# Kernel tuning notes

Measured on AMD Instinct MI355X. Metric: run time of the kernel, lower is better.

Reference implementation:

```python
import jax, jax.numpy as jnp
import numpy as np

VOCAB, EMBED = 100000, 128
B, QLEN, DLEN = 1024, 32, 256
KERNEL_NUM, SIGMA, EXACT_SIGMA = 11, 0.1, 0.001
EPS = 1e-8  # torch F.cosine_similarity eps


def _kernel_mus(n):
    l_mu = [1.0]
    if n == 1:
        return l_mu
    bin_size = 2.0 / (n - 1)
    l_mu.append(1 - bin_size / 2)
    for i in range(1, n - 1):
        l_mu.append(round(l_mu[i] - bin_size, 5))
    return list(reversed(l_mu))


def _kernel_sigmas(n, sigma, exact_sigma):
    l_sigma = [exact_sigma]
    if n == 1:
        return l_sigma
    l_sigma += [sigma] * (n - 1)
    return list(reversed(l_sigma))


MUS = jnp.asarray(np.array(_kernel_mus(KERNEL_NUM), dtype=np.float32))      # [K]
SIGMAS = jnp.asarray(np.array(_kernel_sigmas(KERNEL_NUM, SIGMA, EXACT_SIGMA), dtype=np.float32))  # [K]


def setup_inputs() -> dict:
    key = jax.random.key(0)
    k = jax.random.split(key, 7)
    return {
        "emb": jax.random.normal(k[0], (VOCAB, EMBED), dtype=jnp.float32),
        "mlp_w": jax.random.normal(k[1], (1, KERNEL_NUM), dtype=jnp.float32) * 0.3,
        "mlp_b": jax.random.normal(k[2], (1,), dtype=jnp.float32) * 0.1,
        "query1": jax.random.randint(k[3], (B, QLEN), 0, VOCAB, dtype=jnp.int32).astype(jnp.int64),
        "doc1": jax.random.randint(k[4], (B, DLEN), 0, VOCAB, dtype=jnp.int32).astype(jnp.int64),
        "query2": jax.random.randint(k[5], (B, QLEN), 0, VOCAB, dtype=jnp.int32).astype(jnp.int64),
        "doc2": jax.random.randint(k[6], (B, DLEN), 0, VOCAB, dtype=jnp.int32).astype(jnp.int64),
    }


def _predict(emb, mlp_w, mlp_b, query, doc):
    qe = emb[query]                               # [B,Q,E]
    de = emb[doc]                                 # [B,D,E]
    qn = jnp.linalg.norm(qe, axis=-1)             # [B,Q]
    dn = jnp.linalg.norm(de, axis=-1)             # [B,D]
    dots = jnp.einsum("bqe,bde->bqd", qe, de)    # [B,Q,D]
    sim = dots / jnp.maximum(qn[:, :, None] * dn[:, None, :], EPS)
    # multi-Gaussian soft histogram: exp(-(sim-mu)^2/(2 sigma^2)), sum over doc,
    # log1p, sum over query  -> [B,K]
    z = (sim[..., None] - MUS) / SIGMAS           # [B,Q,D,K]
    K = jnp.exp(-0.5 * z * z)
    pooled = jnp.log1p(K.sum(axis=2)).sum(axis=1)  # [B,K]
    return pooled @ mlp_w.T + mlp_b               # [B,1]


def reference(emb, mlp_w, mlp_b, query1, doc1, query2, doc2):
    logits_1 = _predict(emb, mlp_w, mlp_b, query1, doc1)
    logits_2 = _predict(emb, mlp_w, mlp_b, query2, doc2)
    return jax.nn.sigmoid(logits_1 - logits_2)    # [B,1]
```

## Files before the change

kernel.cpp:

```cpp
#include <hip/hip_runtime.h>
#include <math.h>

#define VOCAB 100000
#define NB    1024
#define QLEN  32
#define DLEN  256
#define EMBED 128
#define KNUM  11

typedef __attribute__((ext_vector_type(8))) short bf16x8;
typedef __attribute__((ext_vector_type(4))) float f32x4;

#define HALF_L2E 0.7213475204444817f
#define TWO_L2E  2.8853900817779268f
#define EM4      0.018315638888734179f

#define SSTR 66
#define SREG (32 * SSTR)

__global__ __launch_bounds__(256)
void cvt_table(const float* __restrict__ emb, ushort* __restrict__ ebf,
               float* __restrict__ inorm)
{
    const int row  = blockIdx.x * 4 + (threadIdx.x >> 6);
    const int lane = threadIdx.x & 63;
    const float2 v = *((const float2*)(emb + (size_t)row * EMBED) + lane);
    union { float f; unsigned u; } a, b;
    a.f = v.x; b.f = v.y;
    const unsigned ra = a.u + 0x8000u;
    const unsigned rb = b.u + 0x8000u;
    *((unsigned*)(ebf + (size_t)row * EMBED) + lane) = (ra >> 16) | (rb & 0xFFFF0000u);
    a.u = ra & 0xFFFF0000u; b.u = rb & 0xFFFF0000u;
    float n = a.f * a.f + b.f * b.f;
    #pragma unroll
    for (int m = 1; m < 64; m <<= 1) n += __shfl_xor(n, m);
    if (lane == 0) inorm[row] = __builtin_amdgcn_rsqf(n);
}

__device__ __forceinline__ bf16x8 cvt8(const float* p, float& nacc)
{
    uint4 a = *((const uint4*)p);
    uint4 b = *((const uint4*)(p + 4));
    unsigned u[8] = {a.x, a.y, a.z, a.w, b.x, b.y, b.z, b.w};
    bf16x8 r;
    #pragma unroll
    for (int i = 0; i < 8; ++i) {
        const unsigned q = u[i] + 0x8000u;
        r[i] = (short)(q >> 16);
        union { unsigned uu; float ff; } g; g.uu = q & 0xFFFF0000u;
        nacc = fmaf(g.ff, g.ff, nacc);
    }
    return r;
}

template<bool PRE>
__global__ __launch_bounds__(256)
void knrm_logits(const float* __restrict__ emb,
                 const ushort* __restrict__ ebf,
                 const float* __restrict__ inorm,
                 const float* __restrict__ mlp_w,
                 const int* __restrict__ q1, const int* __restrict__ d1,
                 const int* __restrict__ q2, const int* __restrict__ d2,
                 float* __restrict__ logits)
{
    const int b    = blockIdx.x;
    const int pair = blockIdx.y;
    const int t    = threadIdx.x;
    const int w    = t >> 6;
    const int lane = t & 63;
    const int l15  = lane & 15;
    const int quad = lane >> 4;

    const int* __restrict__ qry = (pair == 0 ? q1 : q2) + b * QLEN;
    const int* __restrict__ doc = (pair == 0 ? d1 : d2) + b * DLEN;

    __shared__ float s_sim[4 * SREG];
    __shared__ float s_part[4][QLEN][KNUM];

    const int qid0 = qry[l15];
    const int qid1 = qry[l15 + 16];
    int did[4];
    #pragma unroll
    for (int nt = 0; nt < 4; ++nt) did[nt] = doc[(w * 4 + nt) * 16 + l15];

    f32x4 acc[2][4];
    #pragma unroll
    for (int mt = 0; mt < 2; ++mt)
        #pragma unroll
        for (int nt = 0; nt < 4; ++nt)
            acc[mt][nt] = (f32x4){0.f, 0.f, 0.f, 0.f};

    float idn[4];
    float riqn[2][4];

    if (PRE) {
        const ushort* qp0 = ebf + (size_t)qid0 * EMBED + quad * 8;
        const ushort* qp1 = ebf + (size_t)qid1 * EMBED + quad * 8;
        #pragma unroll
        for (int kk = 0; kk < 4; ++kk) {
            const bf16x8 a0 = *((const bf16x8*)(qp0 + kk * 32));
            const bf16x8 a1 = *((const bf16x8*)(qp1 + kk * 32));
            #pragma unroll
            for (int nt = 0; nt < 4; ++nt) {
                const bf16x8 bb = *((const bf16x8*)(ebf + (size_t)did[nt] * EMBED + quad * 8 + kk * 32));
                acc[0][nt] = __builtin_amdgcn_mfma_f32_16x16x32_bf16(a0, bb, acc[0][nt], 0, 0, 0);
                acc[1][nt] = __builtin_amdgcn_mfma_f32_16x16x32_bf16(a1, bb, acc[1][nt], 0, 0, 0);
            }
        }
        #pragma unroll
        for (int nt = 0; nt < 4; ++nt) idn[nt] = inorm[did[nt]];
        #pragma unroll
        for (int r = 0; r < 4; ++r) {
            riqn[0][r] = inorm[qry[quad * 4 + r]];
            riqn[1][r] = inorm[qry[16 + quad * 4 + r]];
        }
    } else {
        float qn2[2] = {0.f, 0.f};
        float dn2[4] = {0.f, 0.f, 0.f, 0.f};
        const float* qp0 = emb + (size_t)qid0 * EMBED + quad * 8;
        const float* qp1 = emb + (size_t)qid1 * EMBED + quad * 8;
        #pragma unroll
        for (int kk = 0; kk < 4; ++kk) {
            const bf16x8 a0 = cvt8(qp0 + kk * 32, qn2[0]);
            const bf16x8 a1 = cvt8(qp1 + kk * 32, qn2[1]);
            #pragma unroll
            for (int nt = 0; nt < 4; ++nt) {
                const bf16x8 bb = cvt8(emb + (size_t)did[nt] * EMBED + quad * 8 + kk * 32, dn2[nt]);
                acc[0][nt] = __builtin_amdgcn_mfma_f32_16x16x32_bf16(a0, bb, acc[0][nt], 0, 0, 0);
                acc[1][nt] = __builtin_amdgcn_mfma_f32_16x16x32_bf16(a1, bb, acc[1][nt], 0, 0, 0);
            }
        }
        #pragma unroll
        for (int i = 0; i < 2; ++i) {
            qn2[i] += __shfl_xor(qn2[i], 16);
            qn2[i] += __shfl_xor(qn2[i], 32);
        }
        #pragma unroll
        for (int nt = 0; nt < 4; ++nt) {
            dn2[nt] += __shfl_xor(dn2[nt], 16);
            dn2[nt] += __shfl_xor(dn2[nt], 32);
            idn[nt] = __builtin_amdgcn_rsqf(dn2[nt]);
        }
        #pragma unroll
        for (int r = 0; r < 4; ++r) {
            riqn[0][r] = __builtin_amdgcn_rsqf(__shfl(qn2[0], quad * 4 + r));
            riqn[1][r] = __builtin_amdgcn_rsqf(__shfl(qn2[1], quad * 4 + r));
        }
    }

    {
        float* base = s_sim + w * SREG + (quad * 4) * SSTR + l15;
        #pragma unroll
        for (int mt = 0; mt < 2; ++mt)
            #pragma unroll
            for (int nt = 0; nt < 4; ++nt)
                #pragma unroll
                for (int r = 0; r < 4; ++r)
                    base[(mt * 16 + r) * SSTR + nt * 16] =
                        acc[mt][nt][r] * riqn[mt][r] * idn[nt];
    }
    __syncthreads();

    const int m   = t & 31;
    const int j   = t >> 5;
    const float* rdp = s_sim + (j >> 1) * SREG + m * SSTR + (j & 1);

    float ksum[KNUM];
    #pragma unroll
    for (int k = 0; k < KNUM; ++k) ksum[k] = 0.f;

    #pragma unroll
    for (int i = 0; i < 32; ++i) {
        const float s  = rdp[2 * i];
        const float z  = fmaf(s, 10.f, -1.f);
        const float e0 = exp2f(-HALF_L2E * (z * z));
        float ru = exp2f(fmaf(z,  TWO_L2E, -TWO_L2E));
        float rd = exp2f(fmaf(z, -TWO_L2E, -TWO_L2E));
        ksum[5] += e0;
        float tt = e0;
        tt *= ru; ksum[6] += tt; ru *= EM4;
        tt *= ru; ksum[7] += tt; ru *= EM4;
        tt *= ru; ksum[8] += tt; ru *= EM4;
        tt *= ru; ksum[9] += tt;
        tt = e0;
        tt *= rd; ksum[4] += tt; rd *= EM4;
        tt *= rd; ksum[3] += tt; rd *= EM4;
        tt *= rd; ksum[2] += tt; rd *= EM4;
        tt *= rd; ksum[1] += tt; rd *= EM4;
        tt *= rd; ksum[0] += tt;
        ksum[10] += (s > 0.995f) ? 1.f : 0.f;
    }

    #pragma unroll
    for (int k = 0; k < KNUM; ++k) ksum[k] += __shfl_xor(ksum[k], 32);

    if (lane < 32) {
        #pragma unroll
        for (int k = 0; k < KNUM; ++k) s_part[w][m][k] = ksum[k];
    }
    __syncthreads();

    if (t < QLEN) {
        float contrib = 0.f;
        #pragma unroll
        for (int k = 0; k < KNUM; ++k) {
            const float ks = s_part[0][t][k] + s_part[1][t][k]
                           + s_part[2][t][k] + s_part[3][t][k];
            contrib += mlp_w[k] * log1pf(ks);
        }
        #pragma unroll
        for (int mm = 1; mm < 32; mm <<= 1) contrib += __shfl_xor(contrib, mm);
        if (t == 0) logits[pair * NB + b] = contrib;
    }
}

__global__ __launch_bounds__(256)
void knrm_combine(const float* __restrict__ logits, float* __restrict__ out)
{
    const int i = blockIdx.x * blockDim.x + threadIdx.x;
    if (i < NB) {
        const float d = logits[i] - logits[NB + i];
        out[i] = 1.f / (1.f + __expf(-d));
    }
}

extern "C" void kernel_launch(void* const* d_in, const int* in_sizes, int n_in,
                              void* d_out, int out_size, void* d_ws, size_t ws_size,
                              hipStream_t stream)
{
    const float* emb   = (const float*)d_in[0];
    const float* mlp_w = (const float*)d_in[1];
    const int* q1 = (const int*)d_in[3];
    const int* d1 = (const int*)d_in[4];
    const int* q2 = (const int*)d_in[5];
    const int* d2 = (const int*)d_in[6];

    float* out    = (float*)d_out;
    float* logits = (float*)d_ws;

    const size_t need = 2 * NB * 4
                      + (size_t)VOCAB * 4
                      + (size_t)VOCAB * EMBED * 2 + 256;
    dim3 grid(NB, 2);
    if (ws_size >= need) {
        float*  inorm = logits + 2 * NB;
        ushort* ebf   = (ushort*)(inorm + VOCAB);
        cvt_table<<<VOCAB / 4, 256, 0, stream>>>(emb, ebf, inorm);
        knrm_logits<true><<<grid, 256, 0, stream>>>(emb, ebf, inorm, mlp_w,
                                                    q1, d1, q2, d2, logits);
    } else {
        knrm_logits<false><<<grid, 256, 0, stream>>>(emb, nullptr, nullptr, mlp_w,
                                                     q1, d1, q2, d2, logits);
    }
    knrm_combine<<<(NB + 255) / 256, 256, 0, stream>>>(logits, out);
}
```

Baseline: 146.8 us.

## Shrink similarity LDS tile to per-wave halves and reduce kernels via shared atomics

The main kernel no longer stages the full 32x64 similarity tile per wave. Each wave now writes one 16-row half at a time and evaluates the Gaussian kernels on it straight away. Partial sums are reduced with wave shuffles and LDS atomics into one shared total, which drops the second block-wide barrier over a large tile and cuts LDS use. Together with a launch-bounds occupancy hint, this aims to fit more blocks per CU. The table conversion kernel also now processes 8 rows per block with float4 loads. The costs are an extra barrier to zero the totals, LDS atomic contention, and possible register pressure from the occupancy hint.

```diff
diff --git a/kernel.cpp b/kernel.cpp
--- a/kernel.cpp
+++ b/kernel.cpp
@@ -15,26 +15,30 @@
 #define TWO_L2E  2.8853900817779268f
 #define EM4      0.018315638888734179f
 
-#define SSTR 66
-#define SREG (32 * SSTR)
+#define SSTR  68
+#define SHALF (16 * SSTR)
 
 __global__ __launch_bounds__(256)
 void cvt_table(const float* __restrict__ emb, ushort* __restrict__ ebf,
                float* __restrict__ inorm)
 {
-    const int row  = blockIdx.x * 4 + (threadIdx.x >> 6);
-    const int lane = threadIdx.x & 63;
-    const float2 v = *((const float2*)(emb + (size_t)row * EMBED) + lane);
-    union { float f; unsigned u; } a, b;
-    a.f = v.x; b.f = v.y;
-    const unsigned ra = a.u + 0x8000u;
-    const unsigned rb = b.u + 0x8000u;
-    *((unsigned*)(ebf + (size_t)row * EMBED) + lane) = (ra >> 16) | (rb & 0xFFFF0000u);
-    a.u = ra & 0xFFFF0000u; b.u = rb & 0xFFFF0000u;
-    float n = a.f * a.f + b.f * b.f;
-    #pragma unroll
-    for (int m = 1; m < 64; m <<= 1) n += __shfl_xor(n, m);
-    if (lane == 0) inorm[row] = __builtin_amdgcn_rsqf(n);
+    const int row = blockIdx.x * 8 + (threadIdx.x >> 5);
+    const int l32 = threadIdx.x & 31;
+    const float4 v = *((const float4*)(emb + (size_t)row * EMBED) + l32);
+    union { float f; unsigned u; } x0, x1, x2, x3;
+    x0.f = v.x; x1.f = v.y; x2.f = v.z; x3.f = v.w;
+    const unsigned r0 = x0.u + 0x8000u, r1 = x1.u + 0x8000u;
+    const unsigned r2 = x2.u + 0x8000u, r3 = x3.u + 0x8000u;
+    uint2 packed;
+    packed.x = (r0 >> 16) | (r1 & 0xFFFF0000u);
+    packed.y = (r2 >> 16) | (r3 & 0xFFFF0000u);
+    *((uint2*)(ebf + (size_t)row * EMBED) + l32) = packed;
+    x0.u = r0 & 0xFFFF0000u; x1.u = r1 & 0xFFFF0000u;
+    x2.u = r2 & 0xFFFF0000u; x3.u = r3 & 0xFFFF0000u;
+    float n = x0.f * x0.f + x1.f * x1.f + x2.f * x2.f + x3.f * x3.f;
+    #pragma unroll
+    for (int m = 1; m < 32; m <<= 1) n += __shfl_xor(n, m);
+    if (l32 == 0) inorm[row] = __builtin_amdgcn_rsqf(n);
 }
 
 __device__ __forceinline__ bf16x8 cvt8(const float* p, float& nacc)
@@ -54,7 +58,7 @@
 }
 
 template<bool PRE>
-__global__ __launch_bounds__(256)
+__global__ __launch_bounds__(256, 6)
 void knrm_logits(const float* __restrict__ emb,
                  const ushort* __restrict__ ebf,
                  const float* __restrict__ inorm,
@@ -74,8 +78,12 @@
     const int* __restrict__ qry = (pair == 0 ? q1 : q2) + b * QLEN;
     const int* __restrict__ doc = (pair == 0 ? d1 : d2) + b * DLEN;
 
-    __shared__ float s_sim[4 * SREG];
-    __shared__ float s_part[4][QLEN][KNUM];
+    __shared__ __align__(16) float s_sim[4 * SHALF];
+    __shared__ float s_tot[QLEN][12];
+
+    #pragma unroll
+    for (int i = t; i < QLEN * 12; i += 256) ((float*)s_tot)[i] = 0.f;
+    __syncthreads();
 
     const int qid0 = qry[l15];
     const int qid1 = qry[l15 + 16];
@@ -148,66 +156,68 @@
         }
     }
 
-    {
-        float* base = s_sim + w * SREG + (quad * 4) * SSTR + l15;
-        #pragma unroll
-        for (int mt = 0; mt < 2; ++mt)
-            #pragma unroll
-            for (int nt = 0; nt < 4; ++nt)
-                #pragma unroll
-                for (int r = 0; r < 4; ++r)
-                    base[(mt * 16 + r) * SSTR + nt * 16] =
-                        acc[mt][nt][r] * riqn[mt][r] * idn[nt];
-    }
-    __syncthreads();
-
-    const int m   = t & 31;
-    const int j   = t >> 5;
-    const float* rdp = s_sim + (j >> 1) * SREG + m * SSTR + (j & 1);
-
-    float ksum[KNUM];
-    #pragma unroll
-    for (int k = 0; k < KNUM; ++k) ksum[k] = 0.f;
-
-    #pragma unroll
-    for (int i = 0; i < 32; ++i) {
-        const float s  = rdp[2 * i];
-        const float z  = fmaf(s, 10.f, -1.f);
-        const float e0 = exp2f(-HALF_L2E * (z * z));
-        float ru = exp2f(fmaf(z,  TWO_L2E, -TWO_L2E));
-        float rd = exp2f(fmaf(z, -TWO_L2E, -TWO_L2E));
-        ksum[5] += e0;
-        float tt = e0;
-        tt *= ru; ksum[6] += tt; ru *= EM4;
-        tt *= ru; ksum[7] += tt; ru *= EM4;
-        tt *= ru; ksum[8] += tt; ru *= EM4;
-        tt *= ru; ksum[9] += tt;
-        tt = e0;
-        tt *= rd; ksum[4] += tt; rd *= EM4;
-        tt *= rd; ksum[3] += tt; rd *= EM4;
-        tt *= rd; ksum[2] += tt; rd *= EM4;
-        tt *= rd; ksum[1] += tt; rd *= EM4;
-        tt *= rd; ksum[0] += tt;
-        ksum[10] += (s > 0.995f) ? 1.f : 0.f;
-    }
-
-    #pragma unroll
-    for (int k = 0; k < KNUM; ++k) ksum[k] += __shfl_xor(ksum[k], 32);
-
-    if (lane < 32) {
-        #pragma unroll
-        for (int k = 0; k < KNUM; ++k) s_part[w][m][k] = ksum[k];
+    float* wtile = s_sim + w * SHALF;
+    const int m = l15;
+    const int c = quad;
+
+    #pragma unroll
+    for (int mt = 0; mt < 2; ++mt) {
+        #pragma unroll
+        for (int nt = 0; nt < 4; ++nt)
+            #pragma unroll
+            for (int r = 0; r < 4; ++r)
+                wtile[(quad * 4 + r) * SSTR + nt * 16 + l15] =
+                    acc[mt][nt][r] * riqn[mt][r] * idn[nt];
+
+        const float* rp = wtile + m * SSTR + c * 16;
+        float ksum[KNUM];
+        #pragma unroll
+        for (int k = 0; k < KNUM; ++k) ksum[k] = 0.f;
+
+        #pragma unroll
+        for (int i = 0; i < 4; ++i) {
+            const f32x4 sv = *((const f32x4*)(rp + 4 * i));
+            #pragma unroll
+            for (int e = 0; e < 4; ++e) {
+                const float s  = sv[e];
+                const float z  = fmaf(s, 10.f, -1.f);
+                const float e0 = exp2f(-HALF_L2E * (z * z));
+                float ru = exp2f(fmaf(z,  TWO_L2E, -TWO_L2E));
+                float rd = exp2f(fmaf(z, -TWO_L2E, -TWO_L2E));
+                ksum[5] += e0;
+                float tt = e0;
+                tt *= ru; ksum[6] += tt; ru *= EM4;
+                tt *= ru; ksum[7] += tt; ru *= EM4;
+                tt *= ru; ksum[8] += tt; ru *= EM4;
+                tt *= ru; ksum[9] += tt;
+                tt = e0;
+                tt *= rd; ksum[4] += tt; rd *= EM4;
+                tt *= rd; ksum[3] += tt; rd *= EM4;
+                tt *= rd; ksum[2] += tt; rd *= EM4;
+                tt *= rd; ksum[1] += tt; rd *= EM4;
+                tt *= rd; ksum[0] += tt;
+                ksum[10] += (s > 0.995f) ? 1.f : 0.f;
+            }
+        }
+
+        #pragma unroll
+        for (int k = 0; k < KNUM; ++k) {
+            ksum[k] += __shfl_xor(ksum[k], 16);
+            ksum[k] += __shfl_xor(ksum[k], 32);
+        }
+        if (quad == 0) {
+            #pragma unroll
+            for (int k = 0; k < KNUM; ++k)
+                atomicAdd(&s_tot[mt * 16 + m][k], ksum[k]);
+        }
     }
     __syncthreads();
 
     if (t < QLEN) {
         float contrib = 0.f;
         #pragma unroll
-        for (int k = 0; k < KNUM; ++k) {
-            const float ks = s_part[0][t][k] + s_part[1][t][k]
-                           + s_part[2][t][k] + s_part[3][t][k];
-            contrib += mlp_w[k] * log1pf(ks);
-        }
+        for (int k = 0; k < KNUM; ++k)
+            contrib += mlp_w[k] * log1pf(s_tot[t][k]);
         #pragma unroll
         for (int mm = 1; mm < 32; mm <<= 1) contrib += __shfl_xor(contrib, mm);
         if (t == 0) logits[pair * NB + b] = contrib;
@@ -245,7 +255,7 @@
     if (ws_size >= need) {
         float*  inorm = logits + 2 * NB;
         ushort* ebf   = (ushort*)(inorm + VOCAB);
-        cvt_table<<<VOCAB / 4, 256, 0, stream>>>(emb, ebf, inorm);
+        cvt_table<<<VOCAB / 8, 256, 0, stream>>>(emb, ebf, inorm);
         knrm_logits<true><<<grid, 256, 0, stream>>>(emb, ebf, inorm, mlp_w,
                                                     q1, d1, q2, d2, logits);
     } else {
```

New measurement: 152.7 us. 4.0% more time.
